# Kernel optimization log

Hardware: AMD Instinct MI355X
Metric: run time of the kernel (lower is better)

Reference implementation:

```python
import jax, jax.numpy as jnp
import numpy as np

B, L, D = 8, 8192, 512


def setup_inputs() -> dict:
    key = jax.random.key(0)
    ks = jax.random.split(key, 8)
    sc = 1.0 / np.sqrt(D).astype(np.float32)
    return {
        "emotion_h": jax.random.normal(ks[0], (B, 1, D), jnp.float32),
        "sents_h": jax.random.normal(ks[1], (B, L, D), jnp.float32),
        "pre_sents_h": jax.random.normal(ks[2], (B, L, D), jnp.float32),
        "pos_sents_h": jax.random.normal(ks[3], (B, L, D), jnp.float32),
        "W1": jax.random.normal(ks[4], (D, D), jnp.float32) * sc,
        "b1": jnp.zeros((D,), jnp.float32),
        "W2": jax.random.normal(ks[5], (D, D), jnp.float32) * sc,
        "b2": jnp.zeros((D,), jnp.float32),
        "W3": jax.random.normal(ks[6], (D, 1), jnp.float32) * sc,
        "b3": jnp.zeros((1,), jnp.float32),
    }


def reference(emotion_h, sents_h, pre_sents_h, pos_sents_h, W1, b1, W2, b2, W3, b3):
    # Attention: score over sentences conditioned on emotion vector.
    eq = emotion_h @ W1 + b1                      # (B, 1, D)
    sq = sents_h @ W2 + b2                        # (B, L, D)
    logits = (jnp.tanh(eq + sq) @ W3 + b3)[..., 0]  # (B, L)
    s = jax.nn.softmax(logits, axis=-1)           # (B, L), sums to 1 over L

    # Original builds (B,L,3,L) tril/eye/triu masks and matmuls with the
    # expanded score -> per-position weights are:
    #   pre_w[i]  = sum_{j<i} s[j]   (tril(-1))
    #   self_w[i] = s[i]             (eye)
    #   pos_w[i]  = sum_{j>i} s[j]   (triu(+1))
    # Equivalent O(L) form via cumsum:
    c = jnp.cumsum(s, axis=-1)                    # inclusive prefix sum
    pre_w = (c - s)[..., None]                    # exclusive prefix sum
    self_w = s[..., None]
    pos_w = (1.0 - c)[..., None]                  # suffix sum (softmax sums to 1)

    # Weighted combine of the three contexts: sum over the 3-context axis.
    return pre_w * pre_sents_h + self_w * sents_h + pos_w * pos_sents_h
```

## Files before the change

kernel.cpp:

```cpp
#include <hip/hip_runtime.h>
#include <hip/hip_bf16.h>

typedef __bf16 v8bf __attribute__((ext_vector_type(8)));
typedef float  v4f  __attribute__((ext_vector_type(4)));

__device__ __forceinline__ float fast_tanh(float x) {
    x = fminf(fmaxf(x, -15.f), 15.f);
    float t = __builtin_amdgcn_exp2f(x * 2.885390081777927f);
    return (t - 1.f) * __builtin_amdgcn_rcpf(t + 1.f);
}

__global__ __launch_bounds__(256) void k01_prep(const float* __restrict__ W2,
                                                __bf16* __restrict__ w2f,
                                                const float* __restrict__ emo,
                                                const float* __restrict__ W1,
                                                const float* __restrict__ b1,
                                                const float* __restrict__ b2,
                                                float* __restrict__ eqc,
                                                float* __restrict__ logits) {
    if (blockIdx.x < 128) {
        int tid = blockIdx.x * 256 + threadIdx.x;
        int ctg  = tid >> 10;
        int kt   = (tid >> 6) & 15;
        int lane = tid & 63;
        int quad = lane >> 4, col = lane & 15;
        int n = ctg * 16 + col;
        int kbase = kt * 32 + quad * 8;
        v8bf v;
#pragma unroll
        for (int j = 0; j < 8; ++j) v[j] = (__bf16)W2[(kbase + j) * 512 + n];
        *(v8bf*)&w2f[(size_t)tid * 8] = v;
    } else {
        int b = blockIdx.x - 128, t = threadIdx.x;
#pragma unroll
        for (int i = 0; i < 32; ++i) logits[(b * 256 + t) * 32 + i] = 0.f;

        __shared__ float emos[512];
        emos[t]       = emo[b * 512 + t];
        emos[t + 256] = emo[b * 512 + t + 256];
        __syncthreads();
#pragma unroll
        for (int rep = 0; rep < 2; ++rep) {
            int d = t + rep * 256;
            float acc = 0.f;
            for (int k = 0; k < 512; ++k) acc += emos[k] * W1[k * 512 + d];
            eqc[b * 512 + d] = acc + b1[d] + b2[d];
        }
    }
}

__global__ __launch_bounds__(256, 2) void k2_logits(const float* __restrict__ sents,
                                                    const __bf16* __restrict__ w2f,
                                                    const float* __restrict__ eqc,
                                                    const float* __restrict__ W3,
                                                    float* __restrict__ logits) {
    __shared__ __bf16 As[64 * 512];
    const int t = threadIdx.x;
    const int row0 = blockIdx.x * 64;
    const int bidx = row0 >> 13;

#pragma unroll
    for (int it = 0; it < 16; ++it) {
        int idx = t + it * 256;
        int r = idx >> 6, c = idx & 63;
        const float4* src = (const float4*)&sents[(size_t)(row0 + r) * 512 + (c << 3)];
        float4 f0 = src[0], f1 = src[1];
        v8bf v;
        v[0] = (__bf16)f0.x; v[1] = (__bf16)f0.y; v[2] = (__bf16)f0.z; v[3] = (__bf16)f0.w;
        v[4] = (__bf16)f1.x; v[5] = (__bf16)f1.y; v[6] = (__bf16)f1.z; v[7] = (__bf16)f1.w;
        *(v8bf*)&As[r * 512 + ((c ^ (r & 15)) << 3)] = v;
    }
    __syncthreads();

    const int wave = t >> 6, lane = t & 63;
    const int quad = lane >> 4, lcol = lane & 15;
    const int row_half = wave >> 1, col_half = wave & 1;
    const int rbase_local = row_half * 32;

    v4f acc[8][4];
#pragma unroll
    for (int ct = 0; ct < 8; ++ct)
#pragma unroll
        for (int q = 0; q < 4; ++q) acc[ct][q] = (v4f){0.f, 0.f, 0.f, 0.f};

    const __bf16* arow = &As[(rbase_local + lcol) * 512];

    for (int kt = 0; kt < 16; ++kt) {
        const int sc = ((kt * 4 + quad) ^ lcol) << 3;
        v8bf a0 = *(const v8bf*)(arow + sc);
        v8bf a1 = *(const v8bf*)(arow + 16 * 512 + sc);
#pragma unroll
        for (int ct = 0; ct < 8; ++ct) {
            const int ctg = (col_half * 8 + ct) * 2;
            const __bf16* bp = &w2f[(size_t)((ctg * 16 + kt) * 64 + lane) * 8];
            v8bf b0 = *(const v8bf*)bp;
            v8bf b1 = *(const v8bf*)(bp + 16 * 64 * 8);
            acc[ct][0] = __builtin_amdgcn_mfma_f32_16x16x32_bf16(a0, b0, acc[ct][0], 0, 0, 0);
            acc[ct][1] = __builtin_amdgcn_mfma_f32_16x16x32_bf16(a0, b1, acc[ct][1], 0, 0, 0);
            acc[ct][2] = __builtin_amdgcn_mfma_f32_16x16x32_bf16(a1, b0, acc[ct][2], 0, 0, 0);
            acc[ct][3] = __builtin_amdgcn_mfma_f32_16x16x32_bf16(a1, b1, acc[ct][3], 0, 0, 0);
        }
    }

    float rowacc[8] = {0.f, 0.f, 0.f, 0.f, 0.f, 0.f, 0.f, 0.f};
#pragma unroll
    for (int ct = 0; ct < 8; ++ct) {
        const int c0 = (col_half * 8 + ct) * 32;
        float e0  = eqc[bidx * 512 + c0 + lcol];
        float e1  = eqc[bidx * 512 + c0 + 16 + lcol];
        float w30 = W3[c0 + lcol];
        float w31 = W3[c0 + 16 + lcol];
#pragma unroll
        for (int i = 0; i < 4; ++i) {
            rowacc[i]     += fast_tanh(e0 + acc[ct][0][i]) * w30
                           + fast_tanh(e1 + acc[ct][1][i]) * w31;
            rowacc[4 + i] += fast_tanh(e0 + acc[ct][2][i]) * w30
                           + fast_tanh(e1 + acc[ct][3][i]) * w31;
        }
    }
#pragma unroll
    for (int off = 1; off < 16; off <<= 1)
#pragma unroll
        for (int i = 0; i < 8; ++i) rowacc[i] += __shfl_xor(rowacc[i], off, 16);

    if (lcol == 0) {
        int rbase = row0 + rbase_local + quad * 4;
#pragma unroll
        for (int i = 0; i < 4; ++i) {
            atomicAdd(&logits[rbase + i], rowacc[i]);
            atomicAdd(&logits[rbase + 16 + i], rowacc[4 + i]);
        }
    }
}

__global__ __launch_bounds__(1024) void k3_softmax(const float* __restrict__ logits,
                                                   float* __restrict__ sw,
                                                   float* __restrict__ cw) {
    int b = blockIdx.x, t = threadIdx.x;
    const float* lg = logits + b * 8192;
    float v[8];
    float m = -1e30f;
#pragma unroll
    for (int i = 0; i < 8; ++i) { v[i] = lg[t * 8 + i]; m = fmaxf(m, v[i]); }
    __shared__ float red[1024];
    red[t] = m; __syncthreads();
    for (int s = 512; s > 0; s >>= 1) {
        if (t < s) red[t] = fmaxf(red[t], red[t + s]);
        __syncthreads();
    }
    float M = red[0]; __syncthreads();
    float sum = 0.f;
#pragma unroll
    for (int i = 0; i < 8; ++i) {
        v[i] = __builtin_amdgcn_exp2f((v[i] - M) * 1.4426950408889634f);
        sum += v[i];
    }
    red[t] = sum; __syncthreads();
    for (int off = 1; off < 1024; off <<= 1) {
        float add = (t >= off) ? red[t - off] : 0.f;
        __syncthreads();
        red[t] += add;
        __syncthreads();
    }
    float total = red[1023];
    float excl = red[t] - sum;
    float inv = 1.f / total;
    float run = excl;
#pragma unroll
    for (int i = 0; i < 8; ++i) {
        run += v[i];
        sw[b * 8192 + t * 8 + i] = v[i] * inv;
        cw[b * 8192 + t * 8 + i] = run * inv;
    }
}

__global__ __launch_bounds__(256) void k4_combine(const float* __restrict__ sents,
                                                  const float* __restrict__ pre,
                                                  const float* __restrict__ pos,
                                                  const float* __restrict__ sw,
                                                  const float* __restrict__ cw,
                                                  float* __restrict__ out) {
    const size_t stride = (size_t)gridDim.x * 256;
    for (size_t g = (size_t)blockIdx.x * 256 + threadIdx.x; g < 8388608ull; g += stride) {
        size_t base = g << 2;
        int row = (int)(g >> 7);
        float s = sw[row], c = cw[row];
        float pw = c - s, qw = 1.0f - c;
        v4f a = *(const v4f*)&sents[base];
        v4f p = __builtin_nontemporal_load((const v4f*)&pre[base]);
        v4f q = __builtin_nontemporal_load((const v4f*)&pos[base]);
        v4f o = pw * p + s * a + qw * q;
        __builtin_nontemporal_store(o, (v4f*)&out[base]);
    }
}

extern "C" void kernel_launch(void* const* d_in, const int* in_sizes, int n_in,
                              void* d_out, int out_size, void* d_ws, size_t ws_size,
                              hipStream_t stream) {
    const float* emo   = (const float*)d_in[0];
    const float* sents = (const float*)d_in[1];
    const float* pre   = (const float*)d_in[2];
    const float* pos   = (const float*)d_in[3];
    const float* W1    = (const float*)d_in[4];
    const float* b1    = (const float*)d_in[5];
    const float* W2    = (const float*)d_in[6];
    const float* b2    = (const float*)d_in[7];
    const float* W3    = (const float*)d_in[8];
    float* out = (float*)d_out;

    char* ws = (char*)d_ws;
    __bf16* w2f   = (__bf16*)ws;
    float* eqc    = (float*)(ws + 524288);
    float* logits = (float*)(ws + 540672);
    float* sw     = (float*)(ws + 802816);
    float* cw     = (float*)(ws + 1064960);

    k01_prep<<<136, 256, 0, stream>>>(W2, w2f, emo, W1, b1, b2, eqc, logits);
    k2_logits<<<1024, 256, 0, stream>>>(sents, w2f, eqc, W3, logits);
    k3_softmax<<<8, 1024, 0, stream>>>(logits, sw, cw);
    k4_combine<<<2048, 256, 0, stream>>>(sents, pre, pos, sw, cw, out);
}
```

Baseline: 530.6 us.

## Load A operand directly from global, drop LDS staging and logit atomics

The logits GEMM kernel no longer stages the 64x512 bf16 A tile in shared memory. Each lane now loads its fp32 A fragments straight from global memory and converts them in registers, which frees 64KB of LDS and should allow more blocks per CU. The two column-half waves now combine their partial row sums through a small LDS buffer and write logits directly instead of using atomics, so the zero-init of logits is removed. The eq projection in the prep kernel is split across more blocks, each using a K-split reduction. The trade-off is that A rows are re-read from global or L2 by both column-half waves, and the access pattern is strided per lane.

After: 477.3 us. 1.11x faster.

```diff
diff --git a/kernel.cpp b/kernel.cpp
--- a/kernel.cpp
+++ b/kernel.cpp
@@ -8,6 +8,13 @@
     x = fminf(fmaxf(x, -15.f), 15.f);
     float t = __builtin_amdgcn_exp2f(x * 2.885390081777927f);
     return (t - 1.f) * __builtin_amdgcn_rcpf(t + 1.f);
+}
+
+__device__ __forceinline__ v8bf cvt8(float4 f0, float4 f1) {
+    v8bf v;
+    v[0] = (__bf16)f0.x; v[1] = (__bf16)f0.y; v[2] = (__bf16)f0.z; v[3] = (__bf16)f0.w;
+    v[4] = (__bf16)f1.x; v[5] = (__bf16)f1.y; v[6] = (__bf16)f1.z; v[7] = (__bf16)f1.w;
+    return v;
 }
 
 __global__ __launch_bounds__(256) void k01_prep(const float* __restrict__ W2,
@@ -16,8 +23,7 @@
                                                 const float* __restrict__ W1,
                                                 const float* __restrict__ b1,
                                                 const float* __restrict__ b2,
-                                                float* __restrict__ eqc,
-                                                float* __restrict__ logits) {
+                                                float* __restrict__ eqc) {
     if (blockIdx.x < 128) {
         int tid = blockIdx.x * 256 + threadIdx.x;
         int ctg  = tid >> 10;
@@ -31,20 +37,22 @@
         for (int j = 0; j < 8; ++j) v[j] = (__bf16)W2[(kbase + j) * 512 + n];
         *(v8bf*)&w2f[(size_t)tid * 8] = v;
     } else {
-        int b = blockIdx.x - 128, t = threadIdx.x;
-#pragma unroll
-        for (int i = 0; i < 32; ++i) logits[(b * 256 + t) * 32 + i] = 0.f;
-
-        __shared__ float emos[512];
-        emos[t]       = emo[b * 512 + t];
-        emos[t + 256] = emo[b * 512 + t + 256];
-        __syncthreads();
-#pragma unroll
-        for (int rep = 0; rep < 2; ++rep) {
-            int d = t + rep * 256;
-            float acc = 0.f;
-            for (int k = 0; k < 512; ++k) acc += emos[k] * W1[k * 512 + d];
-            eqc[b * 512 + d] = acc + b1[d] + b2[d];
+        __shared__ float part[4][64];
+        int bb = blockIdx.x - 128;
+        int b = bb >> 3, d0 = (bb & 7) << 6;
+        int t = threadIdx.x;
+        int dl = t & 63, ks = t >> 6;
+        const float* eb = emo + b * 512;
+        float acc = 0.f;
+        int kend = ks * 128 + 128;
+        for (int k = ks * 128; k < kend; ++k)
+            acc += eb[k] * W1[k * 512 + d0 + dl];
+        part[ks][dl] = acc;
+        __syncthreads();
+        if (ks == 0) {
+            int d = d0 + dl;
+            float r = part[0][dl] + part[1][dl] + part[2][dl] + part[3][dl];
+            eqc[b * 512 + d] = r + b1[d] + b2[d];
         }
     }
 }
@@ -54,23 +62,10 @@
                                                     const float* __restrict__ eqc,
                                                     const float* __restrict__ W3,
                                                     float* __restrict__ logits) {
-    __shared__ __bf16 As[64 * 512];
+    __shared__ float part[64];
     const int t = threadIdx.x;
     const int row0 = blockIdx.x * 64;
     const int bidx = row0 >> 13;
-
-#pragma unroll
-    for (int it = 0; it < 16; ++it) {
-        int idx = t + it * 256;
-        int r = idx >> 6, c = idx & 63;
-        const float4* src = (const float4*)&sents[(size_t)(row0 + r) * 512 + (c << 3)];
-        float4 f0 = src[0], f1 = src[1];
-        v8bf v;
-        v[0] = (__bf16)f0.x; v[1] = (__bf16)f0.y; v[2] = (__bf16)f0.z; v[3] = (__bf16)f0.w;
-        v[4] = (__bf16)f1.x; v[5] = (__bf16)f1.y; v[6] = (__bf16)f1.z; v[7] = (__bf16)f1.w;
-        *(v8bf*)&As[r * 512 + ((c ^ (r & 15)) << 3)] = v;
-    }
-    __syncthreads();
 
     const int wave = t >> 6, lane = t & 63;
     const int quad = lane >> 4, lcol = lane & 15;
@@ -83,12 +78,17 @@
 #pragma unroll
         for (int q = 0; q < 4; ++q) acc[ct][q] = (v4f){0.f, 0.f, 0.f, 0.f};
 
-    const __bf16* arow = &As[(rbase_local + lcol) * 512];
-
+    const float* a0p = &sents[(size_t)(row0 + rbase_local + lcol) * 512 + quad * 8];
+    const float* a1p = a0p + 16 * 512;
+
+#pragma unroll 2
     for (int kt = 0; kt < 16; ++kt) {
-        const int sc = ((kt * 4 + quad) ^ lcol) << 3;
-        v8bf a0 = *(const v8bf*)(arow + sc);
-        v8bf a1 = *(const v8bf*)(arow + 16 * 512 + sc);
+        const float4* p0 = (const float4*)(a0p + kt * 32);
+        const float4* p1 = (const float4*)(a1p + kt * 32);
+        float4 f00 = p0[0], f01 = p0[1];
+        float4 f10 = p1[0], f11 = p1[1];
+        v8bf a0 = cvt8(f00, f01);
+        v8bf a1 = cvt8(f10, f11);
 #pragma unroll
         for (int ct = 0; ct < 8; ++ct) {
             const int ctg = (col_half * 8 + ct) * 2;
@@ -123,12 +123,20 @@
 #pragma unroll
         for (int i = 0; i < 8; ++i) rowacc[i] += __shfl_xor(rowacc[i], off, 16);
 
-    if (lcol == 0) {
-        int rbase = row0 + rbase_local + quad * 4;
+    const int rl = rbase_local + quad * 4;
+    if (col_half == 1 && lcol == 0) {
 #pragma unroll
         for (int i = 0; i < 4; ++i) {
-            atomicAdd(&logits[rbase + i], rowacc[i]);
-            atomicAdd(&logits[rbase + 16 + i], rowacc[4 + i]);
+            part[rl + i]      = rowacc[i];
+            part[rl + 16 + i] = rowacc[4 + i];
+        }
+    }
+    __syncthreads();
+    if (col_half == 0 && lcol == 0) {
+#pragma unroll
+        for (int i = 0; i < 4; ++i) {
+            logits[row0 + rl + i]      = rowacc[i]     + part[rl + i];
+            logits[row0 + rl + 16 + i] = rowacc[4 + i] + part[rl + 16 + i];
         }
     }
 }
@@ -215,7 +223,7 @@
     float* sw     = (float*)(ws + 802816);
     float* cw     = (float*)(ws + 1064960);
 
-    k01_prep<<<136, 256, 0, stream>>>(W2, w2f, emo, W1, b1, b2, eqc, logits);
+    k01_prep<<<192, 256, 0, stream>>>(W2, w2f, emo, W1, b1, b2, eqc);
     k2_logits<<<1024, 256, 0, stream>>>(sents, w2f, eqc, W3, logits);
     k3_softmax<<<8, 1024, 0, stream>>>(logits, sw, cw);
     k4_combine<<<2048, 256, 0, stream>>>(sents, pre, pos, sw, cw, out);
```
